# Kernel optimization log

Measured on AMD Instinct MI355X. Metric: run time of the kernel, lower is better.

Reference implementation:

```python
import jax, jax.numpy as jnp
import numpy as np

N, E, H, W, K = 16, 128, 128, 128, 8  # batch, num_experts, height, width, top-k


def setup_inputs() -> dict:
    key = jax.random.key(0)
    k1, k2, k3 = jax.random.split(key, 3)
    return {
        "x": jax.random.normal(k1, (N, E, H, W), dtype=jnp.float32),        # unused by forward math (kept for signature fidelity)
        "experts": jax.random.normal(k2, (N, E, H, W), dtype=jnp.float32),  # per-expert output maps
        "gate_w": jax.random.normal(k3, (E, E), dtype=jnp.float32) * 0.05,  # 1x1 gating projection (out, in)
        "gate_b": jnp.zeros((E,), dtype=jnp.float32),
    }


def reference(x, experts, gate_w, gate_b):
    # Gate: 1x1 conv over the expert-channel dim -> per-pixel routing logits, then softmax.
    logits = jnp.einsum('nehw,fe->nfhw', experts, gate_w) + gate_b[None, :, None, None]
    routing_weights = jax.nn.softmax(logits, axis=1)  # [N, E, H, W]

    # SMoERouting: per-pixel top-k expert selection, gather expert values, scale by gate weight.
    rw_t = jnp.transpose(routing_weights, (0, 2, 3, 1))       # [N, H, W, E]
    top_vals, top_idx = jax.lax.top_k(rw_t, K)                # [N, H, W, K]
    experts_t = jnp.transpose(experts, (0, 2, 3, 1))          # [N, H, W, E]
    gathered = jnp.take_along_axis(experts_t, top_idx, axis=-1)  # irregular gather [N, H, W, K]
    selected = gathered * top_vals
    return jnp.transpose(selected, (0, 3, 1, 2))              # [N, K, H, W]
```

## Files before the change

### kernel.cpp

```cpp
#include <hip/hip_runtime.h>
#include <math.h>

#define NB 16
#define NE 128
#define NK 8
#define HW 16384
#define NPIX (NB * HW)

__device__ float g_gwT[NE * NE];

__global__ __launch_bounds__(256) void cvt_gw_kernel(const float* __restrict__ gate_w) {
    int i = blockIdx.x * 256 + threadIdx.x;
    if (i < NE * NE) {
        int e = i >> 7;
        int f = i & 127;
        g_gwT[i] = gate_w[f * NE + e];
    }
}

__global__ __launch_bounds__(256) void moe_kernel(const float* __restrict__ experts,
                                                  const float* __restrict__ gate_b,
                                                  float* __restrict__ out) {
    const int p  = blockIdx.x * 256 + threadIdx.x;
    const int n  = p >> 14;
    const int hw = p & (HW - 1);

    const float* xp = experts + ((size_t)n * NE * HW + hw);

    float acc[NE];
#pragma unroll
    for (int f = 0; f < NE; ++f) acc[f] = 0.0f;

    for (int e = 0; e < NE; ++e) {
        float xe = xp[(size_t)e * HW];
        const float* gw = &g_gwT[e * NE];
#pragma unroll
        for (int f = 0; f < NE; ++f) {
            acc[f] = fmaf(gw[f], xe, acc[f]);
        }
    }

#pragma unroll
    for (int f = 0; f < NE; ++f) acc[f] = acc[f] + gate_b[f];

    float m = acc[0];
#pragma unroll
    for (int f = 1; f < NE; ++f) m = fmaxf(m, acc[f]);

#pragma unroll
    for (int f = 0; f < NE; ++f) {
        acc[f] = (float)exp((double)(acc[f] - m));
    }

    float s = acc[0];
#pragma unroll
    for (int f = 1; f < NE; ++f) s = s + acc[f];

#pragma unroll
    for (int f = 0; f < NE; ++f) acc[f] = acc[f] / s;

    float t_v[NK];
    int   t_i[NK];
#pragma unroll
    for (int i = 0; i < NK; ++i) { t_v[i] = -1.0f; t_i[i] = 0; }

#pragma unroll
    for (int f = 0; f < NE; ++f) {
        float v  = acc[f];
        int   ix = f;
#pragma unroll
        for (int i = 0; i < NK; ++i) {
            bool gt = v > t_v[i];
            float tv = t_v[i]; int ti = t_i[i];
            t_v[i] = gt ? v  : tv;
            t_i[i] = gt ? ix : ti;
            v      = gt ? tv : v;
            ix     = gt ? ti : ix;
        }
    }

    float* op = out + ((size_t)n * NK * HW + hw);
#pragma unroll
    for (int k = 0; k < NK; ++k) {
        float xv = xp[(size_t)t_i[k] * HW];
        op[(size_t)k * HW] = t_v[k] * xv;
    }
}

extern "C" void kernel_launch(void* const* d_in, const int* in_sizes, int n_in,
                              void* d_out, int out_size, void* d_ws, size_t ws_size,
                              hipStream_t stream) {
    const float* experts = (const float*)d_in[1];
    const float* gate_w  = (const float*)d_in[2];
    const float* gate_b  = (const float*)d_in[3];
    float* out = (float*)d_out;

    hipLaunchKernelGGL(cvt_gw_kernel, dim3((NE * NE + 255) / 256), dim3(256), 0, stream, gate_w);
    hipLaunchKernelGGL(moe_kernel, dim3(NPIX / 256), dim3(256), 0, stream, experts, gate_b, out);
}
```

Baseline: 287.2 us.

## Broadcast gate weights via readlane and prefetch expert inputs in groups

```diff
diff --git a/kernel.cpp b/kernel.cpp
--- a/kernel.cpp
+++ b/kernel.cpp
@@ -7,7 +7,7 @@
 #define HW 16384
 #define NPIX (NB * HW)
 
-__device__ float g_gwT[NE * NE];
+__device__ __align__(16) float g_gwT[NE * NE];
 
 __global__ __launch_bounds__(256) void cvt_gw_kernel(const float* __restrict__ gate_w) {
     int i = blockIdx.x * 256 + threadIdx.x;
@@ -18,25 +18,74 @@
     }
 }
 
+#define PAIR_COMPUTE(GBUF, XE0, XE1)                                                     \
+    {                                                                                    \
+        _Pragma("unroll")                                                                \
+        for (int j = 0; j < 32; ++j) {                                                   \
+            float w0 = __int_as_float(__builtin_amdgcn_readlane(__float_as_int(GBUF.x), j)); \
+            float w1 = __int_as_float(__builtin_amdgcn_readlane(__float_as_int(GBUF.y), j)); \
+            float w2 = __int_as_float(__builtin_amdgcn_readlane(__float_as_int(GBUF.z), j)); \
+            float w3 = __int_as_float(__builtin_amdgcn_readlane(__float_as_int(GBUF.w), j)); \
+            acc[4 * j + 0] = fmaf(w0, XE0, acc[4 * j + 0]);                              \
+            acc[4 * j + 1] = fmaf(w1, XE0, acc[4 * j + 1]);                              \
+            acc[4 * j + 2] = fmaf(w2, XE0, acc[4 * j + 2]);                              \
+            acc[4 * j + 3] = fmaf(w3, XE0, acc[4 * j + 3]);                              \
+        }                                                                                \
+        _Pragma("unroll")                                                                \
+        for (int j = 0; j < 32; ++j) {                                                   \
+            float w0 = __int_as_float(__builtin_amdgcn_readlane(__float_as_int(GBUF.x), 32 + j)); \
+            float w1 = __int_as_float(__builtin_amdgcn_readlane(__float_as_int(GBUF.y), 32 + j)); \
+            float w2 = __int_as_float(__builtin_amdgcn_readlane(__float_as_int(GBUF.z), 32 + j)); \
+            float w3 = __int_as_float(__builtin_amdgcn_readlane(__float_as_int(GBUF.w), 32 + j)); \
+            acc[4 * j + 0] = fmaf(w0, XE1, acc[4 * j + 0]);                              \
+            acc[4 * j + 1] = fmaf(w1, XE1, acc[4 * j + 1]);                              \
+            acc[4 * j + 2] = fmaf(w2, XE1, acc[4 * j + 2]);                              \
+            acc[4 * j + 3] = fmaf(w3, XE1, acc[4 * j + 3]);                              \
+        }                                                                                \
+    }
+
 __global__ __launch_bounds__(256) void moe_kernel(const float* __restrict__ experts,
                                                   const float* __restrict__ gate_b,
                                                   float* __restrict__ out) {
-    const int p  = blockIdx.x * 256 + threadIdx.x;
-    const int n  = p >> 14;
-    const int hw = p & (HW - 1);
+    const int tid  = threadIdx.x;
+    const int lane = tid & 63;
+    const int p    = blockIdx.x * 256 + tid;
+    const int n    = p >> 14;
+    const int hw   = p & (HW - 1);
 
     const float* xp = experts + ((size_t)n * NE * HW + hw);
+
+    const float4* gwq = ((const float4*)g_gwT) + lane;
 
     float acc[NE];
 #pragma unroll
     for (int f = 0; f < NE; ++f) acc[f] = 0.0f;
 
-    for (int e = 0; e < NE; ++e) {
-        float xe = xp[(size_t)e * HW];
-        const float* gw = &g_gwT[e * NE];
+    float xr[8], xn[8];
 #pragma unroll
-        for (int f = 0; f < NE; ++f) {
-            acc[f] = fmaf(gw[f], xe, acc[f]);
+    for (int i = 0; i < 8; ++i) xr[i] = xp[(size_t)i * HW];
+
+    float4 ga = gwq[0];
+    float4 gb;
+
+    for (int g = 0; g < 16; ++g) {
+        if (g < 15) {
+            const float* xq = xp + (size_t)(g + 1) * 8 * HW;
+#pragma unroll
+            for (int i = 0; i < 8; ++i) xn[i] = xq[(size_t)i * HW];
+        }
+        gb = gwq[(size_t)(4 * g + 1) * 64];
+        PAIR_COMPUTE(ga, xr[0], xr[1]);
+        ga = gwq[(size_t)(4 * g + 2) * 64];
+        PAIR_COMPUTE(gb, xr[2], xr[3]);
+        gb = gwq[(size_t)(4 * g + 3) * 64];
+        PAIR_COMPUTE(ga, xr[4], xr[5]);
+        if (4 * g + 4 < 64) ga = gwq[(size_t)(4 * g + 4) * 64];
+        PAIR_COMPUTE(gb, xr[6], xr[7]);
+
+        if (g < 15) {
+#pragma unroll
+            for (int i = 0; i < 8; ++i) xr[i] = xn[i];
         }
     }
 
```

Result: slower. 571.7 us (+99.1%).
